# Optimization experiments

Measured on AMD Instinct MI355X. Metric: run time of the kernel, lower is better.

## Reference

```python
import jax, jax.numpy as jnp
import numpy as np

D_MODEL = 1024
N_HEADS = 16
D_HEAD = D_MODEL // N_HEADS
EPS_LN = 1e-5
EPS_GATE = 1e-5
EPS_DEN = 1e-5


def setup_inputs() -> dict:
    key = jax.random.key(0)
    ks = jax.random.split(key, 4)
    B, T, D = 1, 2048, D_MODEL
    x = jax.random.normal(ks[0], (B, T, D), dtype=jnp.float32)
    # Linear weights scaled like torch default init (~1/sqrt(fan_in))
    s = 1.0 / np.sqrt(D)
    qkv_w = jax.random.normal(ks[1], (3 * D, D), dtype=jnp.float32) * s
    gate_w = jax.random.normal(ks[2], (D, D), dtype=jnp.float32) * s
    proj_w = jax.random.normal(ks[3], (D, D), dtype=jnp.float32) * s
    return {
        "x": x,
        "ln_g": jnp.ones((D,), jnp.float32),
        "ln_b": jnp.zeros((D,), jnp.float32),
        "qkv_w": qkv_w,
        "qkv_b": jnp.zeros((3 * D,), jnp.float32),
        "gate_w": gate_w,
        "gate_b": jnp.zeros((D,), jnp.float32),
        "proj_w": proj_w,
        "proj_b": jnp.zeros((D,), jnp.float32),
    }


def _linear(x, w, b):
    # torch nn.Linear: y = x @ W^T + b, W is (out, in)
    return jnp.einsum("btd,od->bto", x, w) + b


def reference(x, ln_g, ln_b, qkv_w, qkv_b, gate_w, gate_b, proj_w, proj_b):
    B, T, D = x.shape
    H, Dh = N_HEADS, D_HEAD

    # LayerNorm
    mu = jnp.mean(x, axis=-1, keepdims=True)
    var = jnp.mean((x - mu) ** 2, axis=-1, keepdims=True)
    x_norm = (x - mu) / jnp.sqrt(var + EPS_LN) * ln_g + ln_b

    qkv = _linear(x_norm, qkv_w, qkv_b)
    q, k, v = jnp.split(qkv, 3, axis=-1)

    # concept gate on raw x
    gate_sig = jax.nn.sigmoid(_linear(x, gate_w, gate_b))
    gate_norm = gate_sig / (jnp.mean(gate_sig, axis=-1, keepdims=True) + EPS_GATE)
    q = q * gate_norm
    k = k * gate_norm

    # (B,T,D) -> (B,H,T,Dh)
    def heads(t):
        return t.reshape(B, T, H, Dh).transpose(0, 2, 1, 3)

    q, k, v = heads(q).astype(jnp.float32), heads(k).astype(jnp.float32), heads(v).astype(jnp.float32)

    q = jax.nn.elu(q) + 1.0
    k = jax.nn.elu(k) + 1.0

    # causal linear attention via cumsum of outer products (same math as source)
    kv = jnp.einsum("bhtd,bhtm->bhtdm", k, v)        # (B,H,T,Dh,Dh)
    kv_cum = jnp.cumsum(kv, axis=2)
    out_num = jnp.einsum("bhtd,bhtdm->bhtm", q, kv_cum)
    k_cum = jnp.cumsum(k, axis=2)
    out_den = jnp.einsum("bhtd,bhtd->bht", q, k_cum)[..., None] + EPS_DEN
    out = out_num / out_den                           # (B,H,T,Dh)

    out = out.astype(x_norm.dtype).transpose(0, 2, 1, 3).reshape(B, T, D)
    return _linear(out, proj_w, proj_b)
```

## Files before the change

kernel.cpp:

```cpp
#include <hip/hip_runtime.h>
#include <hip/hip_bf16.h>
#include <math.h>

#define T_SEQ 2048
#define DM 1024
#define NH 16
#define DH 64
#define CHUNK 64
#define NCHUNK (T_SEQ / CHUNK)

typedef __hip_bfloat16 bf16;
typedef __attribute__((ext_vector_type(8))) short short8;
typedef __attribute__((ext_vector_type(4))) short short4v;
typedef __attribute__((ext_vector_type(4))) float f32x4;

static __device__ __forceinline__ short f2b_bits(float f) {
  bf16 t = __float2bfloat16(f);
  short s;
  __builtin_memcpy(&s, &t, 2);
  return s;
}
static __device__ __forceinline__ float b2f(short s) {
  unsigned int u = ((unsigned int)(unsigned short)s) << 16;
  float f;
  __builtin_memcpy(&f, &u, 4);
  return f;
}

static __device__ __forceinline__ float gelu1(float raw, float gate, float inv) {
  float x = raw * gate * inv;
  return x > 0.f ? x + 1.f : __expf(x);
}

static __device__ __forceinline__ void gload16(const void* g, void* l) {
  __builtin_amdgcn_global_load_lds((const __attribute__((address_space(1))) void*)g,
                                   (__attribute__((address_space(3))) void*)l, 16, 0, 0);
}

#define PREP_WBLOCKS (5 * DM * DM / 4 / 256)
__global__ __launch_bounds__(256) void prep_kernel(
    const float* __restrict__ x, const float* __restrict__ g,
    const float* __restrict__ b, const float* __restrict__ qkv_w,
    const float* __restrict__ gate_w, const float* __restrict__ proj_w,
    bf16* __restrict__ xn, bf16* __restrict__ xbf,
    bf16* __restrict__ wqkv, bf16* __restrict__ wgate, bf16* __restrict__ wproj,
    float* __restrict__ gate_accum) {
  const int blk = blockIdx.x;
  if (blk < T_SEQ) {
    const int row = blk;
    if (row < 8) gate_accum[row * 256 + threadIdx.x] = 0.f;
    const float* xr = x + (size_t)row * DM;
    float vals[4];
    float s = 0.f, s2 = 0.f;
#pragma unroll
    for (int i = 0; i < 4; i++) {
      float v = xr[threadIdx.x + i * 256];
      vals[i] = v;
      s += v;
      s2 += v * v;
    }
#pragma unroll
    for (int m = 1; m < 64; m <<= 1) {
      s += __shfl_xor(s, m, 64);
      s2 += __shfl_xor(s2, m, 64);
    }
    __shared__ float red[8];
    const int wid = threadIdx.x >> 6;
    if ((threadIdx.x & 63) == 0) {
      red[wid] = s;
      red[4 + wid] = s2;
    }
    __syncthreads();
    s = red[0] + red[1] + red[2] + red[3];
    s2 = red[4] + red[5] + red[6] + red[7];
    const float mean = s * (1.f / DM);
    const float var = s2 * (1.f / DM) - mean * mean;
    const float rstd = rsqrtf(var + 1e-5f);
#pragma unroll
    for (int i = 0; i < 4; i++) {
      int idx = threadIdx.x + i * 256;
      float v = (vals[i] - mean) * rstd * g[idx] + b[idx];
      xn[(size_t)row * DM + idx] = __float2bfloat16(v);
      xbf[(size_t)row * DM + idx] = __float2bfloat16(vals[i]);
    }
  } else {
    constexpr int NQ = 3 * DM * DM / 4, NS = DM * DM / 4;
    int i = (blk - T_SEQ) * 256 + threadIdx.x;
    const float* src;
    bf16* dst;
    int j;
    if (i < NQ) { src = qkv_w; dst = wqkv; j = i; }
    else if (i < NQ + NS) { src = gate_w; dst = wgate; j = i - NQ; }
    else { src = proj_w; dst = wproj; j = i - NQ - NS; }
    float4 v = ((const float4*)src)[j];
    short4v sv;
    sv.x = f2b_bits(v.x); sv.y = f2b_bits(v.y); sv.z = f2b_bits(v.z); sv.w = f2b_bits(v.w);
    *(short4v*)&dst[j * 4] = sv;
  }
}

__global__ __launch_bounds__(256) void gemm_gateqkv(
    const bf16* __restrict__ xbf, const bf16* __restrict__ xn,
    const bf16* __restrict__ wg, const bf16* __restrict__ wq,
    const float* __restrict__ gate_b, const float* __restrict__ qkv_b,
    short* __restrict__ Gb, float* __restrict__ gate_accum,
    short* __restrict__ Qb, short* __restrict__ Kb, short* __restrict__ Vb) {
  constexpr int K = 1024;
  __shared__ __align__(16) short As[2 * 128 * 32];
  __shared__ __align__(16) short Bs[2 * 128 * 32];

  const int tid = threadIdx.x;
  const int wid = tid >> 6, lane = tid & 63;
  const int wm = wid >> 1, wn = wid & 1;
  const int lm = lane & 15, quad = lane >> 4;

  const bool isGate = blockIdx.y < 8;
  const int m0 = blockIdx.x * 128;
  const int n0 = isGate ? blockIdx.y * 128 : (blockIdx.y - 8) * 128;
  const short* Ag = (const short*)(isGate ? xbf : xn);
  const short* Wg = (const short*)(isGate ? wg : wq);

  f32x4 zero = {0.f, 0.f, 0.f, 0.f};
  f32x4 acc[4][4];
#pragma unroll
  for (int i = 0; i < 4; i++)
#pragma unroll
    for (int j = 0; j < 4; j++) acc[i][j] = zero;

  for (int kb = 0; kb < K; kb += 64) {
    __syncthreads();
#pragma unroll
    for (int sec = 0; sec < 2; sec++) {
#pragma unroll
      for (int it = 0; it < 2; it++) {
        const int idx = it * 256 + tid;
        const int row = idx >> 2, seg = (idx & 3) * 8;
        gload16(&Ag[(size_t)(m0 + row) * K + kb + sec * 32 + seg],
                &As[sec * 4096 + (it * 256 + wid * 64) * 8]);
        gload16(&Wg[(size_t)(n0 + row) * K + kb + sec * 32 + seg],
                &Bs[sec * 4096 + (it * 256 + wid * 64) * 8]);
      }
    }
    __syncthreads();
#pragma unroll
    for (int sec = 0; sec < 2; sec++) {
      short8 afr[4], bfr[4];
#pragma unroll
      for (int i = 0; i < 4; i++) {
        afr[i] = *(const short8*)&As[sec * 4096 + (wm * 64 + i * 16 + lm) * 32 + quad * 8];
        bfr[i] = *(const short8*)&Bs[sec * 4096 + (wn * 64 + i * 16 + lm) * 32 + quad * 8];
      }
#pragma unroll
      for (int i = 0; i < 4; i++)
#pragma unroll
        for (int j = 0; j < 4; j++)
          acc[i][j] = __builtin_amdgcn_mfma_f32_16x16x32_bf16(afr[i], bfr[j], acc[i][j], 0, 0, 0);
    }
  }

  if (isGate) {
    float* red = (float*)As;
    __syncthreads();
#pragma unroll
    for (int i = 0; i < 4; i++) {
#pragma unroll
      for (int r = 0; r < 4; r++) {
        const int rowl = wm * 64 + i * 16 + quad * 4 + r;
        const int row = m0 + rowl;
        float rp = 0.f;
#pragma unroll
        for (int j = 0; j < 4; j++) {
          const int col = n0 + wn * 64 + j * 16 + lm;
          float v = acc[i][j][r] + gate_b[col];
          float sig = 1.f / (1.f + __expf(-v));
          Gb[(size_t)row * DM + col] = f2b_bits(sig);
          rp += sig;
        }
        red[rowl * 32 + wn * 16 + lm] = rp;
      }
    }
    __syncthreads();
    if (tid < 128) {
      float s = 0.f;
#pragma unroll
      for (int t2 = 0; t2 < 32; t2++) s += red[tid * 32 + t2];
      atomicAdd(&gate_accum[m0 + tid], s);
    }
  } else {
#pragma unroll
    for (int i = 0; i < 4; i++) {
      const int rbase = m0 + wm * 64 + i * 16 + quad * 4;
#pragma unroll
      for (int j = 0; j < 4; j++) {
        const int col = n0 + wn * 64 + j * 16 + lm;
        const float bval = qkv_b[col];
#pragma unroll
        for (int r = 0; r < 4; r++) {
          const int row = rbase + r;
          const short bv = f2b_bits(acc[i][j][r] + bval);
          if (col < DM) {
            const int d = col;
            Qb[((size_t)(d >> 6) * T_SEQ + row) * DH + (d & 63)] = bv;
          } else if (col < 2 * DM) {
            const int d = col - DM;
            Kb[((size_t)(d >> 6) * T_SEQ + row) * DH + (d & 63)] = bv;
          } else {
            const int d = col - 2 * DM;
            Vb[((size_t)(d >> 6) * T_SEQ + row) * DH + (d & 63)] = bv;
          }
        }
      }
    }
  }
}

__global__ __launch_bounds__(256) void gemm_proj(const bf16* __restrict__ A,
                                                 const bf16* __restrict__ W,
                                                 const float* __restrict__ bias,
                                                 float* __restrict__ Cout) {
  constexpr int K = 1024;
  __shared__ __align__(16) short As[2 * 64 * 32];
  __shared__ __align__(16) short Bs[2 * 128 * 32];

  const int tid = threadIdx.x;
  const int wid = tid >> 6, lane = tid & 63;
  const int wm = wid >> 1, wn = wid & 1;
  const int lm = lane & 15, quad = lane >> 4;

  const int m0 = blockIdx.x * 64;
  const int n0 = blockIdx.y * 128;
  const short* Ag = (const short*)A;
  const short* Wg = (const short*)W;

  f32x4 zero = {0.f, 0.f, 0.f, 0.f};
  f32x4 acc[2][4];
#pragma unroll
  for (int i = 0; i < 2; i++)
#pragma unroll
    for (int j = 0; j < 4; j++) acc[i][j] = zero;

  for (int kb = 0; kb < K; kb += 64) {
    __syncthreads();
#pragma unroll
    for (int sec = 0; sec < 2; sec++) {
      {
        const int row = tid >> 2, seg = (tid & 3) * 8;
        gload16(&Ag[(size_t)(m0 + row) * K + kb + sec * 32 + seg],
                &As[sec * 2048 + (wid * 64) * 8]);
      }
#pragma unroll
      for (int it = 0; it < 2; it++) {
        const int idx = it * 256 + tid;
        const int row = idx >> 2, seg = (idx & 3) * 8;
        gload16(&Wg[(size_t)(n0 + row) * K + kb + sec * 32 + seg],
                &Bs[sec * 4096 + (it * 256 + wid * 64) * 8]);
      }
    }
    __syncthreads();
#pragma unroll
    for (int sec = 0; sec < 2; sec++) {
      short8 afr[2], bfr[4];
#pragma unroll
      for (int i = 0; i < 2; i++)
        afr[i] = *(const short8*)&As[sec * 2048 + (wm * 32 + i * 16 + lm) * 32 + quad * 8];
#pragma unroll
      for (int j = 0; j < 4; j++)
        bfr[j] = *(const short8*)&Bs[sec * 4096 + (wn * 64 + j * 16 + lm) * 32 + quad * 8];
#pragma unroll
      for (int i = 0; i < 2; i++)
#pragma unroll
        for (int j = 0; j < 4; j++)
          acc[i][j] = __builtin_amdgcn_mfma_f32_16x16x32_bf16(afr[i], bfr[j], acc[i][j], 0, 0, 0);
    }
  }
#pragma unroll
  for (int i = 0; i < 2; i++) {
    const int rbase = m0 + wm * 32 + i * 16 + quad * 4;
#pragma unroll
    for (int j = 0; j < 4; j++) {
      const int col = n0 + wn * 64 + j * 16 + lm;
      const float bval = bias[col];
#pragma unroll
      for (int r = 0; r < 4; r++)
        Cout[(size_t)(rbase + r) * DM + col] = acc[i][j][r] + bval;
    }
  }
}

__global__ __launch_bounds__(256, 2) void chunk_sum_mm(const short* __restrict__ Kb,
                                                       const short* __restrict__ Gb,
                                                       const float* __restrict__ ga,
                                                       const short* __restrict__ Vb,
                                                       float* __restrict__ Skv,
                                                       float* __restrict__ Sk) {
  constexpr int STR = 68;
  __shared__ __align__(16) float Ks2[64 * STR];
  __shared__ __align__(16) float Vs2[64 * STR];
  const int b = blockIdx.x;
  const int h = b >> 5, c = b & 31;
  const int tid = threadIdx.x;
  const int ty = tid >> 4, tx = tid & 15;
  const int d0 = ty * 4, m0 = tx * 4;
  const int t0 = c * CHUNK;
  const size_t cb = ((size_t)h * T_SEQ + t0) * DH;
#pragma unroll
  for (int p = 0; p < 4; p++) {
    int f = p * 256 + tid, row = f >> 4, seg = (f & 15) * 4;
    const int t = t0 + row;
    short4v kr = *(const short4v*)&Kb[cb + row * 64 + seg];
    short4v gr = *(const short4v*)&Gb[(size_t)t * DM + h * 64 + seg];
    short4v vr = *(const short4v*)&Vb[cb + row * 64 + seg];
    const float inv = 1.f / (ga[t] * (1.f / DM) + 1e-5f);
    f32x4 kgv, vv;
#pragma unroll
    for (int e = 0; e < 4; e++) {
      kgv[e] = gelu1(b2f(kr[e]), b2f(gr[e]), inv);
      vv[e] = b2f(vr[e]);
    }
    *(f32x4*)&Ks2[row * STR + seg] = kgv;
    *(f32x4*)&Vs2[row * STR + seg] = vv;
  }
  __syncthreads();
  float acc[4][4] = {};
#pragma unroll 4
  for (int s = 0; s < 64; s++) {
    f32x4 kf = *(const f32x4*)&Ks2[s * STR + d0];
    f32x4 vf = *(const f32x4*)&Vs2[s * STR + m0];
#pragma unroll
    for (int i = 0; i < 4; i++)
#pragma unroll
      for (int j = 0; j < 4; j++) acc[i][j] += kf[i] * vf[j];
  }
  float* outp = Skv + (size_t)b * 4096;
#pragma unroll
  for (int i = 0; i < 4; i++) {
    f32x4 o = {acc[i][0], acc[i][1], acc[i][2], acc[i][3]};
    *(f32x4*)&outp[(d0 + i) * 64 + m0] = o;
  }
  if (tid < 64) {
    float ss = 0.f;
#pragma unroll 4
    for (int s = 0; s < 64; s++) ss += Ks2[s * STR + tid];
    Sk[b * 64 + tid] = ss;
  }
}

__global__ __launch_bounds__(256) void scan_excl(float* __restrict__ Skv,
                                                 float* __restrict__ Sk) {
  const int bid = blockIdx.x, tid = threadIdx.x;
  if (bid < 256) {
    const int id = bid * 256 + tid;
    const int h = id >> 12, e = id & 4095;
    float* base = Skv + (size_t)h * NCHUNK * 4096 + e;
    float v[NCHUNK];
#pragma unroll
    for (int c = 0; c < NCHUNK; c++) v[c] = base[(size_t)c * 4096];
    float run = 0.f;
#pragma unroll
    for (int c = 0; c < NCHUNK; c++) {
      float t = v[c];
      base[(size_t)c * 4096] = run;
      run += t;
    }
  } else {
    const int id = (bid - 256) * 256 + tid;
    const int h = id >> 6, e = id & 63;
    float* base = Sk + (size_t)h * NCHUNK * 64 + e;
    float v[NCHUNK];
#pragma unroll
    for (int c = 0; c < NCHUNK; c++) v[c] = base[c * 64];
    float run = 0.f;
#pragma unroll
    for (int c = 0; c < NCHUNK; c++) {
      float t = v[c];
      base[c * 64] = run;
      run += t;
    }
  }
}

__global__ __launch_bounds__(256, 2) void attn_mm(const short* __restrict__ Qb,
                                                  const short* __restrict__ Kb,
                                                  const short* __restrict__ Gb,
                                                  const float* __restrict__ ga,
                                                  const short* __restrict__ Vb,
                                                  const float* __restrict__ Skv,
                                                  const float* __restrict__ Sk,
                                                  bf16* __restrict__ O) {
  constexpr int STR = 68;
  __shared__ __align__(16) float Qs[64 * STR];
  __shared__ __align__(16) float Vs[64 * STR];
  __shared__ __align__(16) float KPs[64 * STR];
  __shared__ float denp[64 * 16];
  __shared__ float skp[64];
  __shared__ float den[64];
  const int b = blockIdx.x;
  const int h = b >> 5, c = b & 31;
  const int tid = threadIdx.x;
  const int ty = tid >> 4, tx = tid & 15;
  const int r0 = ty * 4, c0 = tx * 4, m0 = tx * 4;
  const int t0 = c * CHUNK;
  const size_t cb = ((size_t)h * T_SEQ + t0) * DH;
  const float* Pg = Skv + (size_t)b * 4096;

  short4v kreg[4], greg[4];
  float ireg[4];
#pragma unroll
  for (int p = 0; p < 4; p++) {
    int f = p * 256 + tid, row = f >> 4, seg = (f & 15) * 4;
    kreg[p] = *(const short4v*)&Kb[cb + row * 64 + seg];
    greg[p] = *(const short4v*)&Gb[(size_t)(t0 + row) * DM + h * 64 + seg];
    ireg[p] = 1.f / (ga[t0 + row] * (1.f / DM) + 1e-5f);
  }
#pragma unroll
  for (int p = 0; p < 4; p++) {
    int f = p * 256 + tid, row = f >> 4, seg = (f & 15) * 4;
    short4v qr = *(const short4v*)&Qb[cb + row * 64 + seg];
    short4v gq = *(const short4v*)&Gb[(size_t)(t0 + row) * DM + h * 64 + seg];
    short4v vr = *(const short4v*)&Vb[cb + row * 64 + seg];
    const float inv = 1.f / (ga[t0 + row] * (1.f / DM) + 1e-5f);
    f32x4 qgv, vv;
#pragma unroll
    for (int e = 0; e < 4; e++) {
      qgv[e] = gelu1(b2f(qr[e]), b2f(gq[e]), inv);
      vv[e] = b2f(vr[e]);
    }
    *(f32x4*)&Qs[row * STR + seg] = qgv;
    *(f32x4*)&Vs[row * STR + seg] = vv;
    *(f32x4*)&KPs[row * STR + seg] = *(const f32x4*)&Pg[row * 64 + seg];
  }
  if (tid < 64) skp[tid] = Sk[b * 64 + tid];
  __syncthreads();

  if (tid < 64) {
    float s = 1e-5f;
#pragma unroll 4
    for (int d = 0; d < 64; d++) s += Qs[tid * STR + d] * skp[d];
    den[tid] = s;
  }

  float accO[4][4] = {};
#pragma unroll 2
  for (int d0 = 0; d0 < 64; d0 += 4) {
    f32x4 qf[4], pf[4];
#pragma unroll
    for (int i = 0; i < 4; i++) qf[i] = *(const f32x4*)&Qs[(r0 + i) * STR + d0];
#pragma unroll
    for (int dd = 0; dd < 4; dd++) pf[dd] = *(const f32x4*)&KPs[(d0 + dd) * STR + m0];
#pragma unroll
    for (int i = 0; i < 4; i++)
#pragma unroll
      for (int j = 0; j < 4; j++)
        accO[i][j] += qf[i][0] * pf[0][j] + qf[i][1] * pf[1][j] +
                      qf[i][2] * pf[2][j] + qf[i][3] * pf[3][j];
  }
  __syncthreads();
#pragma unroll
  for (int p = 0; p < 4; p++) {
    int f = p * 256 + tid, row = f >> 4, seg = (f & 15) * 4;
    f32x4 kgv;
#pragma unroll
    for (int e = 0; e < 4; e++) kgv[e] = gelu1(b2f(kreg[p][e]), b2f(greg[p][e]), ireg[p]);
    *(f32x4*)&KPs[row * STR + seg] = kgv;
  }
  __syncthreads();

  float accS[4][4] = {};
#pragma unroll 2
  for (int d0 = 0; d0 < 64; d0 += 4) {
    f32x4 qf[4], kf[4];
#pragma unroll
    for (int i = 0; i < 4; i++) qf[i] = *(const f32x4*)&Qs[(r0 + i) * STR + d0];
#pragma unroll
    for (int j = 0; j < 4; j++) kf[j] = *(const f32x4*)&KPs[(c0 + j) * STR + d0];
#pragma unroll
    for (int i = 0; i < 4; i++)
#pragma unroll
      for (int j = 0; j < 4; j++)
        accS[i][j] += qf[i][0] * kf[j][0] + qf[i][1] * kf[j][1] +
                      qf[i][2] * kf[j][2] + qf[i][3] * kf[j][3];
  }
  float dp[4];
#pragma unroll
  for (int i = 0; i < 4; i++) {
    dp[i] = 0.f;
#pragma unroll
    for (int j = 0; j < 4; j++) {
      float v = (c0 + j) <= (r0 + i) ? accS[i][j] : 0.f;
      accS[i][j] = v;
      dp[i] += v;
    }
  }
  __syncthreads();
#pragma unroll
  for (int i = 0; i < 4; i++) {
    f32x4 sv = {accS[i][0], accS[i][1], accS[i][2], accS[i][3]};
    *(f32x4*)&Qs[(r0 + i) * STR + c0] = sv;
    denp[(r0 + i) * 16 + tx] = dp[i];
  }
  __syncthreads();
  if (tid < 64) {
    float s = den[tid];
#pragma unroll
    for (int t = 0; t < 16; t++) s += denp[tid * 16 + t];
    den[tid] = s;
  }

#pragma unroll 2
  for (int c4 = 0; c4 < 64; c4 += 4) {
    f32x4 sf[4], vf[4];
#pragma unroll
    for (int i = 0; i < 4; i++) sf[i] = *(const f32x4*)&Qs[(r0 + i) * STR + c4];
#pragma unroll
    for (int cc = 0; cc < 4; cc++) vf[cc] = *(const f32x4*)&Vs[(c4 + cc) * STR + m0];
#pragma unroll
    for (int i = 0; i < 4; i++)
#pragma unroll
      for (int j = 0; j < 4; j++)
        accO[i][j] += sf[i][0] * vf[0][j] + sf[i][1] * vf[1][j] +
                      sf[i][2] * vf[2][j] + sf[i][3] * vf[3][j];
  }
  __syncthreads();

#pragma unroll
  for (int i = 0; i < 4; i++) {
    const float inv = 1.f / den[r0 + i];
    short4v ov;
#pragma unroll
    for (int j = 0; j < 4; j++) ov[j] = f2b_bits(accO[i][j] * inv);
    *(short4v*)&O[(size_t)(t0 + r0 + i) * DM + h * 64 + m0] = ov;
  }
}

extern "C" void kernel_launch(void* const* d_in, const int* in_sizes, int n_in,
                              void* d_out, int out_size, void* d_ws, size_t ws_size,
                              hipStream_t stream) {
  (void)in_sizes; (void)n_in; (void)out_size; (void)ws_size;
  const float* x      = (const float*)d_in[0];
  const float* ln_g   = (const float*)d_in[1];
  const float* ln_b   = (const float*)d_in[2];
  const float* qkv_w  = (const float*)d_in[3];
  const float* qkv_b  = (const float*)d_in[4];
  const float* gate_w = (const float*)d_in[5];
  const float* gate_b = (const float*)d_in[6];
  const float* proj_w = (const float*)d_in[7];
  const float* proj_b = (const float*)d_in[8];
  float* out = (float*)d_out;

  char* ws = (char*)d_ws;
  size_t off = 0;
  auto alloc = [&](size_t bytes) {
    void* p = ws + off;
    off += (bytes + 255) & ~(size_t)255;
    return p;
  };
  bf16*  xn       = (bf16*)alloc((size_t)T_SEQ * DM * 2);
  bf16*  xbf      = (bf16*)alloc((size_t)T_SEQ * DM * 2);
  bf16*  wqkv     = (bf16*)alloc((size_t)3 * DM * DM * 2);
  bf16*  wgate    = (bf16*)alloc((size_t)DM * DM * 2);
  bf16*  wproj    = (bf16*)alloc((size_t)DM * DM * 2);
  short* Gb       = (short*)alloc((size_t)T_SEQ * DM * 2);
  float* gate_accum = (float*)alloc((size_t)T_SEQ * 4);
  short* Qb       = (short*)alloc((size_t)T_SEQ * DM * 2);
  short* Kb       = (short*)alloc((size_t)T_SEQ * DM * 2);
  short* Vb       = (short*)alloc((size_t)T_SEQ * DM * 2);
  bf16*  Obuf     = (bf16*)alloc((size_t)T_SEQ * DM * 2);
  float* Skv      = (float*)alloc((size_t)NH * NCHUNK * 4096 * 4);
  float* Sk       = (float*)alloc((size_t)NH * NCHUNK * 64 * 4);

  prep_kernel<<<T_SEQ + PREP_WBLOCKS, 256, 0, stream>>>(
      x, ln_g, ln_b, qkv_w, gate_w, proj_w, xn, xbf, wqkv, wgate, wproj, gate_accum);
  gemm_gateqkv<<<dim3(16, 32), 256, 0, stream>>>(xbf, xn, wgate, wqkv, gate_b, qkv_b,
                                                 Gb, gate_accum, Qb, Kb, Vb);
  chunk_sum_mm<<<NH * NCHUNK, 256, 0, stream>>>(Kb, Gb, gate_accum, Vb, Skv, Sk);
  scan_excl<<<260, 256, 0, stream>>>(Skv, Sk);
  attn_mm<<<NH * NCHUNK, 256, 0, stream>>>(Qb, Kb, Gb, gate_accum, Vb, Skv, Sk, Obuf);
  gemm_proj<<<dim3(32, 8), 256, 0, stream>>>(Obuf, wproj, proj_b, out);
}
```

Measured before the change: 165.8 us.

## Fuse all stages into one cooperative persistent kernel with grid syncs

Merges the six separate kernels (prep, gate/QKV GEMM, chunk sums, scan, attention, projection) into a single cooperative launch of 512 blocks, with grid.sync between phases and a shared-memory union reused across phases. It is meant to remove per-kernel launch and drain gaps. The projection GEMM is retiled to 64x64 tiles so it also fits 512 blocks, and prep becomes a grid-stride loop. The costs are a union-sized LDS footprint that limits occupancy, grid-wide barrier overhead, and a fallback to separate launches if the cooperative launch fails.

Result: slower. 463.5 us (+179.6%).

```diff
diff --git a/kernel.cpp b/kernel.cpp
--- a/kernel.cpp
+++ b/kernel.cpp
@@ -1,6 +1,9 @@
 #include <hip/hip_runtime.h>
+#include <hip/hip_cooperative_groups.h>
 #include <hip/hip_bf16.h>
 #include <math.h>
+
+namespace cg = cooperative_groups;
 
 #define T_SEQ 2048
 #define DM 1024
@@ -8,6 +11,7 @@
 #define DH 64
 #define CHUNK 64
 #define NCHUNK (T_SEQ / CHUNK)
+#define NBLK 512
 
 typedef __hip_bfloat16 bf16;
 typedef __attribute__((ext_vector_type(8))) short short8;
@@ -26,35 +30,45 @@
   __builtin_memcpy(&f, &u, 4);
   return f;
 }
-
 static __device__ __forceinline__ float gelu1(float raw, float gate, float inv) {
   float x = raw * gate * inv;
   return x > 0.f ? x + 1.f : __expf(x);
 }
-
 static __device__ __forceinline__ void gload16(const void* g, void* l) {
   __builtin_amdgcn_global_load_lds((const __attribute__((address_space(1))) void*)g,
                                    (__attribute__((address_space(3))) void*)l, 16, 0, 0);
 }
 
-#define PREP_WBLOCKS (5 * DM * DM / 4 / 256)
-__global__ __launch_bounds__(256) void prep_kernel(
-    const float* __restrict__ x, const float* __restrict__ g,
-    const float* __restrict__ b, const float* __restrict__ qkv_w,
-    const float* __restrict__ gate_w, const float* __restrict__ proj_w,
-    bf16* __restrict__ xn, bf16* __restrict__ xbf,
-    bf16* __restrict__ wqkv, bf16* __restrict__ wgate, bf16* __restrict__ wproj,
-    float* __restrict__ gate_accum) {
-  const int blk = blockIdx.x;
-  if (blk < T_SEQ) {
-    const int row = blk;
-    if (row < 8) gate_accum[row * 256 + threadIdx.x] = 0.f;
-    const float* xr = x + (size_t)row * DM;
+struct P {
+  const float *x, *ln_g, *ln_b, *qkv_w, *qkv_b, *gate_w, *gate_b, *proj_w, *proj_b;
+  bf16 *xn, *xbf, *wqkv, *wgate, *wproj;
+  short *Gb;
+  float *ga;
+  short *Qb, *Kb, *Vb;
+  bf16 *Obuf;
+  float *Skv, *Sk;
+  float *out;
+};
+
+union SH {
+  struct { short A[8192]; short B[8192]; } g;
+  struct { float K[4352]; float V[4352]; } cs;
+  struct { float Q[4352]; float V[4352]; float KP[4352];
+           float denp[1024]; float skp[64]; float den[64]; } at;
+  struct { short A[4096]; short B[4096]; } pj;
+  float lnred[8];
+};
+
+static __device__ void phase_prep(const P& p, int blk, SH& sh) {
+  const int tid = threadIdx.x;
+  if (blk < 8) p.ga[blk * 256 + tid] = 0.f;
+  for (int row = blk; row < T_SEQ; row += NBLK) {
+    const float* xr = p.x + (size_t)row * DM;
     float vals[4];
     float s = 0.f, s2 = 0.f;
 #pragma unroll
     for (int i = 0; i < 4; i++) {
-      float v = xr[threadIdx.x + i * 256];
+      float v = xr[tid + i * 256];
       vals[i] = v;
       s += v;
       s2 += v * v;
@@ -64,34 +78,34 @@
       s += __shfl_xor(s, m, 64);
       s2 += __shfl_xor(s2, m, 64);
     }
-    __shared__ float red[8];
-    const int wid = threadIdx.x >> 6;
-    if ((threadIdx.x & 63) == 0) {
-      red[wid] = s;
-      red[4 + wid] = s2;
-    }
-    __syncthreads();
-    s = red[0] + red[1] + red[2] + red[3];
-    s2 = red[4] + red[5] + red[6] + red[7];
+    const int wid = tid >> 6;
+    if ((tid & 63) == 0) {
+      sh.lnred[wid] = s;
+      sh.lnred[4 + wid] = s2;
+    }
+    __syncthreads();
+    s = sh.lnred[0] + sh.lnred[1] + sh.lnred[2] + sh.lnred[3];
+    s2 = sh.lnred[4] + sh.lnred[5] + sh.lnred[6] + sh.lnred[7];
+    __syncthreads();
     const float mean = s * (1.f / DM);
     const float var = s2 * (1.f / DM) - mean * mean;
     const float rstd = rsqrtf(var + 1e-5f);
 #pragma unroll
     for (int i = 0; i < 4; i++) {
-      int idx = threadIdx.x + i * 256;
-      float v = (vals[i] - mean) * rstd * g[idx] + b[idx];
-      xn[(size_t)row * DM + idx] = __float2bfloat16(v);
-      xbf[(size_t)row * DM + idx] = __float2bfloat16(vals[i]);
-    }
-  } else {
-    constexpr int NQ = 3 * DM * DM / 4, NS = DM * DM / 4;
-    int i = (blk - T_SEQ) * 256 + threadIdx.x;
+      int idx = tid + i * 256;
+      float v = (vals[i] - mean) * rstd * p.ln_g[idx] + p.ln_b[idx];
+      p.xn[(size_t)row * DM + idx] = __float2bfloat16(v);
+      p.xbf[(size_t)row * DM + idx] = __float2bfloat16(vals[i]);
+    }
+  }
+  constexpr int NQ = 3 * DM * DM / 4, NS = DM * DM / 4, N4 = 5 * DM * DM / 4;
+  for (int i = blk * 256 + tid; i < N4; i += NBLK * 256) {
     const float* src;
     bf16* dst;
     int j;
-    if (i < NQ) { src = qkv_w; dst = wqkv; j = i; }
-    else if (i < NQ + NS) { src = gate_w; dst = wgate; j = i - NQ; }
-    else { src = proj_w; dst = wproj; j = i - NQ - NS; }
+    if (i < NQ) { src = p.qkv_w; dst = p.wqkv; j = i; }
+    else if (i < NQ + NS) { src = p.gate_w; dst = p.wgate; j = i - NQ; }
+    else { src = p.proj_w; dst = p.wproj; j = i - NQ - NS; }
     float4 v = ((const float4*)src)[j];
     short4v sv;
     sv.x = f2b_bits(v.x); sv.y = f2b_bits(v.y); sv.z = f2b_bits(v.z); sv.w = f2b_bits(v.w);
@@ -99,26 +113,19 @@
   }
 }
 
-__global__ __launch_bounds__(256) void gemm_gateqkv(
-    const bf16* __restrict__ xbf, const bf16* __restrict__ xn,
-    const bf16* __restrict__ wg, const bf16* __restrict__ wq,
-    const float* __restrict__ gate_b, const float* __restrict__ qkv_b,
-    short* __restrict__ Gb, float* __restrict__ gate_accum,
-    short* __restrict__ Qb, short* __restrict__ Kb, short* __restrict__ Vb) {
+static __device__ void phase_gemm1(const P& p, int blk, SH& sh) {
   constexpr int K = 1024;
-  __shared__ __align__(16) short As[2 * 128 * 32];
-  __shared__ __align__(16) short Bs[2 * 128 * 32];
-
   const int tid = threadIdx.x;
   const int wid = tid >> 6, lane = tid & 63;
   const int wm = wid >> 1, wn = wid & 1;
   const int lm = lane & 15, quad = lane >> 4;
 
-  const bool isGate = blockIdx.y < 8;
-  const int m0 = blockIdx.x * 128;
-  const int n0 = isGate ? blockIdx.y * 128 : (blockIdx.y - 8) * 128;
-  const short* Ag = (const short*)(isGate ? xbf : xn);
-  const short* Wg = (const short*)(isGate ? wg : wq);
+  const int bx = blk & 15, by = blk >> 4;
+  const bool isGate = by < 8;
+  const int m0 = bx * 128;
+  const int n0 = isGate ? by * 128 : (by - 8) * 128;
+  const short* Ag = (const short*)(isGate ? p.xbf : p.xn);
+  const short* Wg = (const short*)(isGate ? p.wgate : p.wqkv);
 
   f32x4 zero = {0.f, 0.f, 0.f, 0.f};
   f32x4 acc[4][4];
@@ -136,9 +143,9 @@
         const int idx = it * 256 + tid;
         const int row = idx >> 2, seg = (idx & 3) * 8;
         gload16(&Ag[(size_t)(m0 + row) * K + kb + sec * 32 + seg],
-                &As[sec * 4096 + (it * 256 + wid * 64) * 8]);
+                &sh.g.A[sec * 4096 + (it * 256 + wid * 64) * 8]);
         gload16(&Wg[(size_t)(n0 + row) * K + kb + sec * 32 + seg],
-                &Bs[sec * 4096 + (it * 256 + wid * 64) * 8]);
+                &sh.g.B[sec * 4096 + (it * 256 + wid * 64) * 8]);
       }
     }
     __syncthreads();
@@ -147,8 +154,8 @@
       short8 afr[4], bfr[4];
 #pragma unroll
       for (int i = 0; i < 4; i++) {
-        afr[i] = *(const short8*)&As[sec * 4096 + (wm * 64 + i * 16 + lm) * 32 + quad * 8];
-        bfr[i] = *(const short8*)&Bs[sec * 4096 + (wn * 64 + i * 16 + lm) * 32 + quad * 8];
+        afr[i] = *(const short8*)&sh.g.A[sec * 4096 + (wm * 64 + i * 16 + lm) * 32 + quad * 8];
+        bfr[i] = *(const short8*)&sh.g.B[sec * 4096 + (wn * 64 + i * 16 + lm) * 32 + quad * 8];
       }
 #pragma unroll
       for (int i = 0; i < 4; i++)
@@ -159,7 +166,7 @@
   }
 
   if (isGate) {
-    float* red = (float*)As;
+    float* red = (float*)sh.g.A;
     __syncthreads();
 #pragma unroll
     for (int i = 0; i < 4; i++) {
@@ -171,9 +178,9 @@
 #pragma unroll
         for (int j = 0; j < 4; j++) {
           const int col = n0 + wn * 64 + j * 16 + lm;
-          float v = acc[i][j][r] + gate_b[col];
+          float v = acc[i][j][r] + p.gate_b[col];
           float sig = 1.f / (1.f + __expf(-v));
-          Gb[(size_t)row * DM + col] = f2b_bits(sig);
+          p.Gb[(size_t)row * DM + col] = f2b_bits(sig);
           rp += sig;
         }
         red[rowl * 32 + wn * 16 + lm] = rp;
@@ -184,7 +191,7 @@
       float s = 0.f;
 #pragma unroll
       for (int t2 = 0; t2 < 32; t2++) s += red[tid * 32 + t2];
-      atomicAdd(&gate_accum[m0 + tid], s);
+      atomicAdd(&p.ga[m0 + tid], s);
     }
   } else {
 #pragma unroll
@@ -193,20 +200,20 @@
 #pragma unroll
       for (int j = 0; j < 4; j++) {
         const int col = n0 + wn * 64 + j * 16 + lm;
-        const float bval = qkv_b[col];
+        const float bval = p.qkv_b[col];
 #pragma unroll
         for (int r = 0; r < 4; r++) {
           const int row = rbase + r;
           const short bv = f2b_bits(acc[i][j][r] + bval);
           if (col < DM) {
             const int d = col;
-            Qb[((size_t)(d >> 6) * T_SEQ + row) * DH + (d & 63)] = bv;
+            p.Qb[((size_t)(d >> 6) * T_SEQ + row) * DH + (d & 63)] = bv;
           } else if (col < 2 * DM) {
             const int d = col - DM;
-            Kb[((size_t)(d >> 6) * T_SEQ + row) * DH + (d & 63)] = bv;
+            p.Kb[((size_t)(d >> 6) * T_SEQ + row) * DH + (d & 63)] = bv;
           } else {
             const int d = col - 2 * DM;
-            Vb[((size_t)(d >> 6) * T_SEQ + row) * DH + (d & 63)] = bv;
+            p.Vb[((size_t)(d >> 6) * T_SEQ + row) * DH + (d & 63)] = bv;
           }
         }
       }
@@ -214,89 +221,8 @@
   }
 }
 
-__global__ __launch_bounds__(256) void gemm_proj(const bf16* __restrict__ A,
-                                                 const bf16* __restrict__ W,
-                                                 const float* __restrict__ bias,
-                                                 float* __restrict__ Cout) {
-  constexpr int K = 1024;
-  __shared__ __align__(16) short As[2 * 64 * 32];
-  __shared__ __align__(16) short Bs[2 * 128 * 32];
-
-  const int tid = threadIdx.x;
-  const int wid = tid >> 6, lane = tid & 63;
-  const int wm = wid >> 1, wn = wid & 1;
-  const int lm = lane & 15, quad = lane >> 4;
-
-  const int m0 = blockIdx.x * 64;
-  const int n0 = blockIdx.y * 128;
-  const short* Ag = (const short*)A;
-  const short* Wg = (const short*)W;
-
-  f32x4 zero = {0.f, 0.f, 0.f, 0.f};
-  f32x4 acc[2][4];
-#pragma unroll
-  for (int i = 0; i < 2; i++)
-#pragma unroll
-    for (int j = 0; j < 4; j++) acc[i][j] = zero;
-
-  for (int kb = 0; kb < K; kb += 64) {
-    __syncthreads();
-#pragma unroll
-    for (int sec = 0; sec < 2; sec++) {
-      {
-        const int row = tid >> 2, seg = (tid & 3) * 8;
-        gload16(&Ag[(size_t)(m0 + row) * K + kb + sec * 32 + seg],
-                &As[sec * 2048 + (wid * 64) * 8]);
-      }
-#pragma unroll
-      for (int it = 0; it < 2; it++) {
-        const int idx = it * 256 + tid;
-        const int row = idx >> 2, seg = (idx & 3) * 8;
-        gload16(&Wg[(size_t)(n0 + row) * K + kb + sec * 32 + seg],
-                &Bs[sec * 4096 + (it * 256 + wid * 64) * 8]);
-      }
-    }
-    __syncthreads();
-#pragma unroll
-    for (int sec = 0; sec < 2; sec++) {
-      short8 afr[2], bfr[4];
-#pragma unroll
-      for (int i = 0; i < 2; i++)
-        afr[i] = *(const short8*)&As[sec * 2048 + (wm * 32 + i * 16 + lm) * 32 + quad * 8];
-#pragma unroll
-      for (int j = 0; j < 4; j++)
-        bfr[j] = *(const short8*)&Bs[sec * 4096 + (wn * 64 + j * 16 + lm) * 32 + quad * 8];
-#pragma unroll
-      for (int i = 0; i < 2; i++)
-#pragma unroll
-        for (int j = 0; j < 4; j++)
-          acc[i][j] = __builtin_amdgcn_mfma_f32_16x16x32_bf16(afr[i], bfr[j], acc[i][j], 0, 0, 0);
-    }
-  }
-#pragma unroll
-  for (int i = 0; i < 2; i++) {
-    const int rbase = m0 + wm * 32 + i * 16 + quad * 4;
-#pragma unroll
-    for (int j = 0; j < 4; j++) {
-      const int col = n0 + wn * 64 + j * 16 + lm;
-      const float bval = bias[col];
-#pragma unroll
-      for (int r = 0; r < 4; r++)
-        Cout[(size_t)(rbase + r) * DM + col] = acc[i][j][r] + bval;
-    }
-  }
-}
-
-__global__ __launch_bounds__(256, 2) void chunk_sum_mm(const short* __restrict__ Kb,
-                                                       const short* __restrict__ Gb,
-                                                       const float* __restrict__ ga,
-                                                       const short* __restrict__ Vb,
-                                                       float* __restrict__ Skv,
-                                                       float* __restrict__ Sk) {
+static __device__ void phase_csum(const P& p, int b, SH& sh) {
   constexpr int STR = 68;
-  __shared__ __align__(16) float Ks2[64 * STR];
-  __shared__ __align__(16) float Vs2[64 * STR];
-  const int b = blockIdx.x;
   const int h = b >> 5, c = b & 31;
   const int tid = threadIdx.x;
   const int ty = tid >> 4, tx = tid & 15;
@@ -304,34 +230,34 @@
   const int t0 = c * CHUNK;
   const size_t cb = ((size_t)h * T_SEQ + t0) * DH;
 #pragma unroll
-  for (int p = 0; p < 4; p++) {
-    int f = p * 256 + tid, row = f >> 4, seg = (f & 15) * 4;
+  for (int q = 0; q < 4; q++) {
+    int f = q * 256 + tid, row = f >> 4, seg = (f & 15) * 4;
     const int t = t0 + row;
-    short4v kr = *(const short4v*)&Kb[cb + row * 64 + seg];
-    short4v gr = *(const short4v*)&Gb[(size_t)t * DM + h * 64 + seg];
-    short4v vr = *(const short4v*)&Vb[cb + row * 64 + seg];
-    const float inv = 1.f / (ga[t] * (1.f / DM) + 1e-5f);
+    short4v kr = *(const short4v*)&p.Kb[cb + row * 64 + seg];
+    short4v gr = *(const short4v*)&p.Gb[(size_t)t * DM + h * 64 + seg];
+    short4v vr = *(const short4v*)&p.Vb[cb + row * 64 + seg];
+    const float inv = 1.f / (p.ga[t] * (1.f / DM) + 1e-5f);
     f32x4 kgv, vv;
 #pragma unroll
     for (int e = 0; e < 4; e++) {
       kgv[e] = gelu1(b2f(kr[e]), b2f(gr[e]), inv);
       vv[e] = b2f(vr[e]);
     }
-    *(f32x4*)&Ks2[row * STR + seg] = kgv;
-    *(f32x4*)&Vs2[row * STR + seg] = vv;
+    *(f32x4*)&sh.cs.K[row * STR + seg] = kgv;
+    *(f32x4*)&sh.cs.V[row * STR + seg] = vv;
   }
   __syncthreads();
   float acc[4][4] = {};
 #pragma unroll 4
   for (int s = 0; s < 64; s++) {
-    f32x4 kf = *(const f32x4*)&Ks2[s * STR + d0];
-    f32x4 vf = *(const f32x4*)&Vs2[s * STR + m0];
+    f32x4 kf = *(const f32x4*)&sh.cs.K[s * STR + d0];
+    f32x4 vf = *(const f32x4*)&sh.cs.V[s * STR + m0];
 #pragma unroll
     for (int i = 0; i < 4; i++)
 #pragma unroll
       for (int j = 0; j < 4; j++) acc[i][j] += kf[i] * vf[j];
   }
-  float* outp = Skv + (size_t)b * 4096;
+  float* outp = p.Skv + (size_t)b * 4096;
 #pragma unroll
   for (int i = 0; i < 4; i++) {
     f32x4 o = {acc[i][0], acc[i][1], acc[i][2], acc[i][3]};
@@ -340,18 +266,18 @@
   if (tid < 64) {
     float ss = 0.f;
 #pragma unroll 4
-    for (int s = 0; s < 64; s++) ss += Ks2[s * STR + tid];
-    Sk[b * 64 + tid] = ss;
-  }
-}
-
-__global__ __launch_bounds__(256) void scan_excl(float* __restrict__ Skv,
-                                                 float* __restrict__ Sk) {
-  const int bid = blockIdx.x, tid = threadIdx.x;
+    for (int s = 0; s < 64; s++) ss += sh.cs.K[s * STR + tid];
+    p.Sk[b * 64 + tid] = ss;
+  }
+  __syncthreads();
+}
+
+static __device__ void phase_scan(const P& p, int bid) {
+  const int tid = threadIdx.x;
   if (bid < 256) {
     const int id = bid * 256 + tid;
     const int h = id >> 12, e = id & 4095;
-    float* base = Skv + (size_t)h * NCHUNK * 4096 + e;
+    float* base = p.Skv + (size_t)h * NCHUNK * 4096 + e;
     float v[NCHUNK];
 #pragma unroll
     for (int c = 0; c < NCHUNK; c++) v[c] = base[(size_t)c * 4096];
@@ -362,10 +288,10 @@
       base[(size_t)c * 4096] = run;
       run += t;
     }
-  } else {
+  } else if (bid < 260) {
     const int id = (bid - 256) * 256 + tid;
     const int h = id >> 6, e = id & 63;
-    float* base = Sk + (size_t)h * NCHUNK * 64 + e;
+    float* base = p.Sk + (size_t)h * NCHUNK * 64 + e;
     float v[NCHUNK];
 #pragma unroll
     for (int c = 0; c < NCHUNK; c++) v[c] = base[c * 64];
@@ -379,64 +305,50 @@
   }
 }
 
-__global__ __launch_bounds__(256, 2) void attn_mm(const short* __restrict__ Qb,
-                                                  const short* __restrict__ Kb,
-                                                  const short* __restrict__ Gb,
-                                                  const float* __restrict__ ga,
-                                                  const short* __restrict__ Vb,
-                                                  const float* __restrict__ Skv,
-                                                  const float* __restrict__ Sk,
-                                                  bf16* __restrict__ O) {
+static __device__ void phase_attn(const P& p, int b, SH& sh) {
   constexpr int STR = 68;
-  __shared__ __align__(16) float Qs[64 * STR];
-  __shared__ __align__(16) float Vs[64 * STR];
-  __shared__ __align__(16) float KPs[64 * STR];
-  __shared__ float denp[64 * 16];
-  __shared__ float skp[64];
-  __shared__ float den[64];
-  const int b = blockIdx.x;
   const int h = b >> 5, c = b & 31;
   const int tid = threadIdx.x;
   const int ty = tid >> 4, tx = tid & 15;
   const int r0 = ty * 4, c0 = tx * 4, m0 = tx * 4;
   const int t0 = c * CHUNK;
   const size_t cb = ((size_t)h * T_SEQ + t0) * DH;
-  const float* Pg = Skv + (size_t)b * 4096;
+  const float* Pg = p.Skv + (size_t)b * 4096;
 
   short4v kreg[4], greg[4];
   float ireg[4];
 #pragma unroll
-  for (int p = 0; p < 4; p++) {
-    int f = p * 256 + tid, row = f >> 4, seg = (f & 15) * 4;
-    kreg[p] = *(const short4v*)&Kb[cb + row * 64 + seg];
-    greg[p] = *(const short4v*)&Gb[(size_t)(t0 + row) * DM + h * 64 + seg];
-    ireg[p] = 1.f / (ga[t0 + row] * (1.f / DM) + 1e-5f);
-  }
-#pragma unroll
-  for (int p = 0; p < 4; p++) {
-    int f = p * 256 + tid, row = f >> 4, seg = (f & 15) * 4;
-    short4v qr = *(const short4v*)&Qb[cb + row * 64 + seg];
-    short4v gq = *(const short4v*)&Gb[(size_t)(t0 + row) * DM + h * 64 + seg];
-    short4v vr = *(const short4v*)&Vb[cb + row * 64 + seg];
-    const float inv = 1.f / (ga[t0 + row] * (1.f / DM) + 1e-5f);
+  for (int q = 0; q < 4; q++) {
+    int f = q * 256 + tid, row = f >> 4, seg = (f & 15) * 4;
+    kreg[q] = *(const short4v*)&p.Kb[cb + row * 64 + seg];
+    greg[q] = *(const short4v*)&p.Gb[(size_t)(t0 + row) * DM + h * 64 + seg];
+    ireg[q] = 1.f / (p.ga[t0 + row] * (1.f / DM) + 1e-5f);
+  }
+#pragma unroll
+  for (int q = 0; q < 4; q++) {
+    int f = q * 256 + tid, row = f >> 4, seg = (f & 15) * 4;
+    short4v qr = *(const short4v*)&p.Qb[cb + row * 64 + seg];
+    short4v gq = *(const short4v*)&p.Gb[(size_t)(t0 + row) * DM + h * 64 + seg];
+    short4v vr = *(const short4v*)&p.Vb[cb + row * 64 + seg];
+    const float inv = 1.f / (p.ga[t0 + row] * (1.f / DM) + 1e-5f);
     f32x4 qgv, vv;
 #pragma unroll
     for (int e = 0; e < 4; e++) {
       qgv[e] = gelu1(b2f(qr[e]), b2f(gq[e]), inv);
       vv[e] = b2f(vr[e]);
     }
-    *(f32x4*)&Qs[row * STR + seg] = qgv;
-    *(f32x4*)&Vs[row * STR + seg] = vv;
-    *(f32x4*)&KPs[row * STR + seg] = *(const f32x4*)&Pg[row * 64 + seg];
-  }
-  if (tid < 64) skp[tid] = Sk[b * 64 + tid];
+    *(f32x4*)&sh.at.Q[row * STR + seg] = qgv;
+    *(f32x4*)&sh.at.V[row * STR + seg] = vv;
+    *(f32x4*)&sh.at.KP[row * STR + seg] = *(const f32x4*)&Pg[row * 64 + seg];
+  }
+  if (tid < 64) sh.at.skp[tid] = p.Sk[b * 64 + tid];
   __syncthreads();
 
   if (tid < 64) {
     float s = 1e-5f;
 #pragma unroll 4
-    for (int d = 0; d < 64; d++) s += Qs[tid * STR + d] * skp[d];
-    den[tid] = s;
+    for (int d = 0; d < 64; d++) s += sh.at.Q[tid * STR + d] * sh.at.skp[d];
+    sh.at.den[tid] = s;
   }
 
   float accO[4][4] = {};
@@ -444,9 +356,9 @@
   for (int d0 = 0; d0 < 64; d0 += 4) {
     f32x4 qf[4], pf[4];
 #pragma unroll
-    for (int i = 0; i < 4; i++) qf[i] = *(const f32x4*)&Qs[(r0 + i) * STR + d0];
-#pragma unroll
-    for (int dd = 0; dd < 4; dd++) pf[dd] = *(const f32x4*)&KPs[(d0 + dd) * STR + m0];
+    for (int i = 0; i < 4; i++) qf[i] = *(const f32x4*)&sh.at.Q[(r0 + i) * STR + d0];
+#pragma unroll
+    for (int dd = 0; dd < 4; dd++) pf[dd] = *(const f32x4*)&sh.at.KP[(d0 + dd) * STR + m0];
 #pragma unroll
     for (int i = 0; i < 4; i++)
 #pragma unroll
@@ -456,12 +368,12 @@
   }
   __syncthreads();
 #pragma unroll
-  for (int p = 0; p < 4; p++) {
-    int f = p * 256 + tid, row = f >> 4, seg = (f & 15) * 4;
+  for (int q = 0; q < 4; q++) {
+    int f = q * 256 + tid, row = f >> 4, seg = (f & 15) * 4;
     f32x4 kgv;
 #pragma unroll
-    for (int e = 0; e < 4; e++) kgv[e] = gelu1(b2f(kreg[p][e]), b2f(greg[p][e]), ireg[p]);
-    *(f32x4*)&KPs[row * STR + seg] = kgv;
+    for (int e = 0; e < 4; e++) kgv[e] = gelu1(b2f(kreg[q][e]), b2f(greg[q][e]), ireg[q]);
+    *(f32x4*)&sh.at.KP[row * STR + seg] = kgv;
   }
   __syncthreads();
 
@@ -470,9 +382,9 @@
   for (int d0 = 0; d0 < 64; d0 += 4) {
     f32x4 qf[4], kf[4];
 #pragma unroll
-    for (int i = 0; i < 4; i++) qf[i] = *(const f32x4*)&Qs[(r0 + i) * STR + d0];
-#pragma unroll
-    for (int j = 0; j < 4; j++) kf[j] = *(const f32x4*)&KPs[(c0 + j) * STR + d0];
+    for (int i = 0; i < 4; i++) qf[i] = *(const f32x4*)&sh.at.Q[(r0 + i) * STR + d0];
+#pragma unroll
+    for (int j = 0; j < 4; j++) kf[j] = *(const f32x4*)&sh.at.KP[(c0 + j) * STR + d0];
 #pragma unroll
     for (int i = 0; i < 4; i++)
 #pragma unroll
@@ -495,24 +407,24 @@
 #pragma unroll
   for (int i = 0; i < 4; i++) {
     f32x4 sv = {accS[i][0], accS[i][1], accS[i][2], accS[i][3]};
-    *(f32x4*)&Qs[(r0 + i) * STR + c0] = sv;
-    denp[(r0 + i) * 16 + tx] = dp[i];
+    *(f32x4*)&sh.at.Q[(r0 + i) * STR + c0] = sv;
+    sh.at.denp[(r0 + i) * 16 + tx] = dp[i];
   }
   __syncthreads();
   if (tid < 64) {
-    float s = den[tid];
-#pragma unroll
-    for (int t = 0; t < 16; t++) s += denp[tid * 16 + t];
-    den[tid] = s;
+    float s = sh.at.den[tid];
+#pragma unroll
+    for (int t = 0; t < 16; t++) s += sh.at.denp[tid * 16 + t];
+    sh.at.den[tid] = s;
   }
 
 #pragma unroll 2
   for (int c4 = 0; c4 < 64; c4 += 4) {
     f32x4 sf[4], vf[4];
 #pragma unroll
-    for (int i = 0; i < 4; i++) sf[i] = *(const f32x4*)&Qs[(r0 + i) * STR + c4];
-#pragma unroll
-    for (int cc = 0; cc < 4; cc++) vf[cc] = *(const f32x4*)&Vs[(c4 + cc) * STR + m0];
+    for (int i = 0; i < 4; i++) sf[i] = *(const f32x4*)&sh.at.Q[(r0 + i) * STR + c4];
+#pragma unroll
+    for (int cc = 0; cc < 4; cc++) vf[cc] = *(const f32x4*)&sh.at.V[(c4 + cc) * STR + m0];
 #pragma unroll
     for (int i = 0; i < 4; i++)
 #pragma unroll
@@ -524,56 +436,145 @@
 
 #pragma unroll
   for (int i = 0; i < 4; i++) {
-    const float inv = 1.f / den[r0 + i];
+    const float inv = 1.f / sh.at.den[r0 + i];
     short4v ov;
 #pragma unroll
     for (int j = 0; j < 4; j++) ov[j] = f2b_bits(accO[i][j] * inv);
-    *(short4v*)&O[(size_t)(t0 + r0 + i) * DM + h * 64 + m0] = ov;
-  }
-}
+    *(short4v*)&p.Obuf[(size_t)(t0 + r0 + i) * DM + h * 64 + m0] = ov;
+  }
+  __syncthreads();
+}
+
+static __device__ void phase_proj(const P& p, int blk, SH& sh) {
+  constexpr int K = 1024;
+  const int tid = threadIdx.x;
+  const int wid = tid >> 6, lane = tid & 63;
+  const int wm = wid >> 1, wn = wid & 1;
+  const int lm = lane & 15, quad = lane >> 4;
+
+  const int m0 = (blk & 31) * 64;
+  const int n0 = (blk >> 5) * 64;
+  const short* Ag = (const short*)p.Obuf;
+  const short* Wg = (const short*)p.wproj;
+
+  f32x4 zero = {0.f, 0.f, 0.f, 0.f};
+  f32x4 acc[2][2];
+#pragma unroll
+  for (int i = 0; i < 2; i++)
+#pragma unroll
+    for (int j = 0; j < 2; j++) acc[i][j] = zero;
+
+  for (int kb = 0; kb < K; kb += 64) {
+    __syncthreads();
+#pragma unroll
+    for (int sec = 0; sec < 2; sec++) {
+      const int row = tid >> 2, seg = (tid & 3) * 8;
+      gload16(&Ag[(size_t)(m0 + row) * K + kb + sec * 32 + seg],
+              &sh.pj.A[sec * 2048 + wid * 512]);
+      gload16(&Wg[(size_t)(n0 + row) * K + kb + sec * 32 + seg],
+              &sh.pj.B[sec * 2048 + wid * 512]);
+    }
+    __syncthreads();
+#pragma unroll
+    for (int sec = 0; sec < 2; sec++) {
+      short8 afr[2], bfr[2];
+#pragma unroll
+      for (int i = 0; i < 2; i++)
+        afr[i] = *(const short8*)&sh.pj.A[sec * 2048 + (wm * 32 + i * 16 + lm) * 32 + quad * 8];
+#pragma unroll
+      for (int j = 0; j < 2; j++)
+        bfr[j] = *(const short8*)&sh.pj.B[sec * 2048 + (wn * 32 + j * 16 + lm) * 32 + quad * 8];
+#pragma unroll
+      for (int i = 0; i < 2; i++)
+#pragma unroll
+        for (int j = 0; j < 2; j++)
+          acc[i][j] = __builtin_amdgcn_mfma_f32_16x16x32_bf16(afr[i], bfr[j], acc[i][j], 0, 0, 0);
+    }
+  }
+#pragma unroll
+  for (int i = 0; i < 2; i++) {
+    const int rbase = m0 + wm * 32 + i * 16 + quad * 4;
+#pragma unroll
+    for (int j = 0; j < 2; j++) {
+      const int col = n0 + wn * 32 + j * 16 + lm;
+      const float bval = p.proj_b[col];
+#pragma unroll
+      for (int r = 0; r < 4; r++)
+        p.out[(size_t)(rbase + r) * DM + col] = acc[i][j][r] + bval;
+    }
+  }
+}
+
+__global__ __launch_bounds__(256, 2) void mega_kernel(P p) {
+  __shared__ __align__(16) SH sh;
+  cg::grid_group grid = cg::this_grid();
+  const int blk = blockIdx.x;
+  phase_prep(p, blk, sh);
+  grid.sync();
+  phase_gemm1(p, blk, sh);
+  grid.sync();
+  phase_csum(p, blk, sh);
+  grid.sync();
+  phase_scan(p, blk);
+  grid.sync();
+  phase_attn(p, blk, sh);
+  grid.sync();
+  phase_proj(p, blk, sh);
+}
+
+__global__ __launch_bounds__(256) void k_prep(P p)  { __shared__ __align__(16) SH sh; phase_prep(p, blockIdx.x, sh); }
+__global__ __launch_bounds__(256) void k_gemm1(P p) { __shared__ __align__(16) SH sh; phase_gemm1(p, blockIdx.x, sh); }
+__global__ __launch_bounds__(256) void k_csum(P p)  { __shared__ __align__(16) SH sh; phase_csum(p, blockIdx.x, sh); }
+__global__ __launch_bounds__(256) void k_scan(P p)  { phase_scan(p, blockIdx.x); }
+__global__ __launch_bounds__(256) void k_attn(P p)  { __shared__ __align__(16) SH sh; phase_attn(p, blockIdx.x, sh); }
+__global__ __launch_bounds__(256) void k_proj(P p)  { __shared__ __align__(16) SH sh; phase_proj(p, blockIdx.x, sh); }
 
 extern "C" void kernel_launch(void* const* d_in, const int* in_sizes, int n_in,
                               void* d_out, int out_size, void* d_ws, size_t ws_size,
                               hipStream_t stream) {
   (void)in_sizes; (void)n_in; (void)out_size; (void)ws_size;
-  const float* x      = (const float*)d_in[0];
-  const float* ln_g   = (const float*)d_in[1];
-  const float* ln_b   = (const float*)d_in[2];
-  const float* qkv_w  = (const float*)d_in[3];
-  const float* qkv_b  = (const float*)d_in[4];
-  const float* gate_w = (const float*)d_in[5];
-  const float* gate_b = (const float*)d_in[6];
-  const float* proj_w = (const float*)d_in[7];
-  const float* proj_b = (const float*)d_in[8];
-  float* out = (float*)d_out;
-
   char* ws = (char*)d_ws;
   size_t off = 0;
   auto alloc = [&](size_t bytes) {
-    void* p = ws + off;
+    void* pp = ws + off;
     off += (bytes + 255) & ~(size_t)255;
-    return p;
+    return pp;
   };
-  bf16*  xn       = (bf16*)alloc((size_t)T_SEQ * DM * 2);
-  bf16*  xbf      = (bf16*)alloc((size_t)T_SEQ * DM * 2);
-  bf16*  wqkv     = (bf16*)alloc((size_t)3 * DM * DM * 2);
-  bf16*  wgate    = (bf16*)alloc((size_t)DM * DM * 2);
-  bf16*  wproj    = (bf16*)alloc((size_t)DM * DM * 2);
-  short* Gb       = (short*)alloc((size_t)T_SEQ * DM * 2);
-  float* gate_accum = (float*)alloc((size_t)T_SEQ * 4);
-  short* Qb       = (short*)alloc((size_t)T_SEQ * DM * 2);
-  short* Kb       = (short*)alloc((size_t)T_SEQ * DM * 2);
-  short* Vb       = (short*)alloc((size_t)T_SEQ * DM * 2);
-  bf16*  Obuf     = (bf16*)alloc((size_t)T_SEQ * DM * 2);
-  float* Skv      = (float*)alloc((size_t)NH * NCHUNK * 4096 * 4);
-  float* Sk       = (float*)alloc((size_t)NH * NCHUNK * 64 * 4);
-
-  prep_kernel<<<T_SEQ + PREP_WBLOCKS, 256, 0, stream>>>(
-      x, ln_g, ln_b, qkv_w, gate_w, proj_w, xn, xbf, wqkv, wgate, wproj, gate_accum);
-  gemm_gateqkv<<<dim3(16, 32), 256, 0, stream>>>(xbf, xn, wgate, wqkv, gate_b, qkv_b,
-                                                 Gb, gate_accum, Qb, Kb, Vb);
-  chunk_sum_mm<<<NH * NCHUNK, 256, 0, stream>>>(Kb, Gb, gate_accum, Vb, Skv, Sk);
-  scan_excl<<<260, 256, 0, stream>>>(Skv, Sk);
-  attn_mm<<<NH * NCHUNK, 256, 0, stream>>>(Qb, Kb, Gb, gate_accum, Vb, Skv, Sk, Obuf);
-  gemm_proj<<<dim3(32, 8), 256, 0, stream>>>(Obuf, wproj, proj_b, out);
-}
+  P p;
+  p.x      = (const float*)d_in[0];
+  p.ln_g   = (const float*)d_in[1];
+  p.ln_b   = (const float*)d_in[2];
+  p.qkv_w  = (const float*)d_in[3];
+  p.qkv_b  = (const float*)d_in[4];
+  p.gate_w = (const float*)d_in[5];
+  p.gate_b = (const float*)d_in[6];
+  p.proj_w = (const float*)d_in[7];
+  p.proj_b = (const float*)d_in[8];
+  p.out    = (float*)d_out;
+  p.xn     = (bf16*)alloc((size_t)T_SEQ * DM * 2);
+  p.xbf    = (bf16*)alloc((size_t)T_SEQ * DM * 2);
+  p.wqkv   = (bf16*)alloc((size_t)3 * DM * DM * 2);
+  p.wgate  = (bf16*)alloc((size_t)DM * DM * 2);
+  p.wproj  = (bf16*)alloc((size_t)DM * DM * 2);
+  p.Gb     = (short*)alloc((size_t)T_SEQ * DM * 2);
+  p.ga     = (float*)alloc((size_t)T_SEQ * 4);
+  p.Qb     = (short*)alloc((size_t)T_SEQ * DM * 2);
+  p.Kb     = (short*)alloc((size_t)T_SEQ * DM * 2);
+  p.Vb     = (short*)alloc((size_t)T_SEQ * DM * 2);
+  p.Obuf   = (bf16*)alloc((size_t)T_SEQ * DM * 2);
+  p.Skv    = (float*)alloc((size_t)NH * NCHUNK * 4096 * 4);
+  p.Sk     = (float*)alloc((size_t)NH * NCHUNK * 64 * 4);
+
+  void* args[] = {&p};
+  hipError_t e = hipLaunchCooperativeKernel((void*)mega_kernel, dim3(NBLK), dim3(256),
+                                            args, 0, stream);
+  if (e != hipSuccess) {
+    (void)hipGetLastError();
+    k_prep<<<NBLK, 256, 0, stream>>>(p);
+    k_gemm1<<<NBLK, 256, 0, stream>>>(p);
+    k_csum<<<NBLK, 256, 0, stream>>>(p);
+    k_scan<<<260, 256, 0, stream>>>(p);
+    k_attn<<<NBLK, 256, 0, stream>>>(p);
+    k_proj<<<NBLK, 256, 0, stream>>>(p);
+  }
+}
```
